# Optimization experiments

Hardware: AMD Instinct MI355X
Metric: run time of the kernel (lower is better)

Reference implementation:

```python
import jax, jax.numpy as jnp
import numpy as np

B, N, D, E, R, K = 4, 2048, 1024, 8, 256, 2


def setup_inputs() -> dict:
    key = jax.random.key(0)
    ks = jax.random.split(key, 5)
    scale = 0.02
    return {
        "x": jax.random.normal(ks[0], (B, N, D), dtype=jnp.float32),
        "gate_w": jax.random.normal(ks[1], (D, E), dtype=jnp.float32) * scale,
        "Wu": jax.random.normal(ks[2], (E, D, R), dtype=jnp.float32) * scale,
        "Wv": jax.random.normal(ks[3], (E, D, R), dtype=jnp.float32) * scale,
        "Wo": jax.random.normal(ks[4], (E, R, D), dtype=jnp.float32) * scale,
    }


def reference(x, gate_w, Wu, Wv, Wo):
    # Router: top-k over expert logits, softmax over the selected k logits.
    logits = jnp.einsum("bnd,de->bne", x, gate_w)          # [B,N,E]
    topv, topi = jax.lax.top_k(logits, K)                    # [B,N,K]
    w = jax.nn.softmax(topv, axis=-1)                        # [B,N,K]

    # Dense all-expert SwiGLU (matches reference semantics: every expert
    # computed for every token, then gathered by top-k index).
    u = jnp.einsum("bnd,edr->bner", x, Wu)                  # [B,N,E,R]
    v = jnp.einsum("bnd,edr->bner", x, Wv)                  # [B,N,E,R]
    s = jax.nn.silu(u) * v                                   # [B,N,E,R]
    Y = jnp.einsum("bner,erd->bned", s, Wo)                 # [B,N,E,D]

    # Gather the k selected experts per token and combine with gate weights.
    y_sel = jnp.take_along_axis(Y, topi[..., None], axis=2)  # [B,N,K,D]
    out = jnp.einsum("bnkd,bnk->bnd", y_sel, w)             # [B,N,D]
    return out
```

## Files before the change

kernel.cpp:

```cpp
#include <hip/hip_runtime.h>
#include <math.h>

#define BN 8192
#define DIM 1024
#define NE 8
#define RR 256

using bf16x8 = __attribute__((ext_vector_type(8))) short;
using f32x4  = __attribute__((ext_vector_type(4))) float;

#define GLD16(g, l) __builtin_amdgcn_global_load_lds(                      \
    (const __attribute__((address_space(1))) void*)(g),                    \
    (__attribute__((address_space(3))) void*)(l), 16, 0, 0)

__device__ inline unsigned short f2bf(float f) {
    unsigned int u = __float_as_uint(f);
    u = (u + 0x7fffu + ((u >> 16) & 1u)) >> 16;
    return (unsigned short)u;
}
__device__ inline float bf2f(unsigned short h) {
    unsigned int u = ((unsigned int)h) << 16;
    return __uint_as_float(u);
}

__global__ __launch_bounds__(256) void k_router3(const float* __restrict__ x,
                                                 const float* __restrict__ gwT,
                                                 int* __restrict__ topi,
                                                 float* __restrict__ topw,
                                                 unsigned short* __restrict__ xb,
                                                 int* __restrict__ counts) {
    __shared__ float gws[NE * DIM];
    __shared__ int bc[NE];
    int tid = threadIdx.x;
    {
        const float4* src = (const float4*)gwT;
        float4* dst = (float4*)gws;
#pragma unroll
        for (int i = 0; i < 8; ++i)
            dst[tid + i * 256] = src[tid + i * 256];
    }
    if (tid < NE) bc[tid] = 0;

    int wid  = (blockIdx.x * blockDim.x + tid) >> 6;
    int lane = tid & 63;
    const float* xp = x + (size_t)wid * DIM + lane * 4;
    unsigned short* xbp = xb + (size_t)wid * DIM + lane * 4;

    float4 xva[4];
#pragma unroll
    for (int k = 0; k < 4; ++k) xva[k] = *(const float4*)(xp + k * 256);

    __syncthreads();

    float4 acc[NE];
#pragma unroll
    for (int e = 0; e < NE; ++e) acc[e] = float4{0.f, 0.f, 0.f, 0.f};
#pragma unroll
    for (int k = 0; k < 4; ++k) {
        float4 xv = xva[k];
#pragma unroll
        for (int e = 0; e < NE; ++e) {
            float4 gv = *(const float4*)(gws + e * DIM + k * 256 + lane * 4);
            acc[e].x += xv.x * gv.x; acc[e].y += xv.y * gv.y;
            acc[e].z += xv.z * gv.z; acc[e].w += xv.w * gv.w;
        }
    }

#pragma unroll
    for (int k = 0; k < 4; ++k) {
        float4 xv = xva[k];
        ushort4 us = { f2bf(xv.x), f2bf(xv.y), f2bf(xv.z), f2bf(xv.w) };
        *(ushort4*)(xbp + k * 256) = us;
    }

    float lg[NE];
#pragma unroll
    for (int e = 0; e < NE; ++e)
        lg[e] = (acc[e].x + acc[e].y) + (acc[e].z + acc[e].w);
#pragma unroll
    for (int off = 32; off; off >>= 1) {
#pragma unroll
        for (int e = 0; e < NE; ++e) lg[e] += __shfl_xor(lg[e], off, 64);
    }
    if (lane == 0) {
        float best = lg[0]; int bi = 0;
#pragma unroll
        for (int e = 1; e < NE; ++e) if (lg[e] > best) { best = lg[e]; bi = e; }
        float sec = -3.4e38f; int si = 0;
#pragma unroll
        for (int e = 0; e < NE; ++e) if (e != bi && lg[e] > sec) { sec = lg[e]; si = e; }
        float p  = __expf(sec - best);
        float w0 = 1.f / (1.f + p);
        float w1 = p * w0;
        topi[wid * 2 + 0] = bi;  topw[wid * 2 + 0] = w0;
        topi[wid * 2 + 1] = si;  topw[wid * 2 + 1] = w1;
        atomicAdd(&bc[bi], 1);
        atomicAdd(&bc[si], 1);
    }
    __syncthreads();
    if (tid < NE) {
        int c = bc[tid];
        if (c) atomicAdd(&counts[tid], c);
    }
}

__global__ __launch_bounds__(256) void k_fill2(const int* __restrict__ topi,
                                               const float* __restrict__ topw,
                                               const int* __restrict__ counts,
                                               int* __restrict__ fill,
                                               int* __restrict__ btok,
                                               float* __restrict__ bw,
                                               int* __restrict__ slotOf) {
    int tid = threadIdx.x;
    int i = blockIdx.x * 256 + tid;
    int w = tid >> 6, lane = tid & 63;
    int e = topi[i];
    float wt = topw[i];

    __shared__ int waveCnt[4][NE];
    __shared__ int wavePre[4][NE];
    __shared__ int baseSh[NE];
    __shared__ int offSh[NE];

    int myrank = 0;
    unsigned long long lt = (1ull << lane) - 1ull;
#pragma unroll
    for (int j = 0; j < NE; ++j) {
        unsigned long long m = __ballot(e == j);
        if (e == j) myrank = __popcll(m & lt);
        if (lane == 0) waveCnt[w][j] = __popcll(m);
    }
    if (tid == 0) {
        int acc = 0;
#pragma unroll
        for (int j = 0; j < NE; ++j) { offSh[j] = acc; acc += counts[j]; }
    }
    __syncthreads();
    if (tid < NE) {
        int j = tid, acc = 0;
#pragma unroll
        for (int ww = 0; ww < 4; ++ww) { wavePre[ww][j] = acc; acc += waveCnt[ww][j]; }
        baseSh[j] = atomicAdd(&fill[j], acc);
    }
    __syncthreads();
    int slot = offSh[e] + baseSh[e] + wavePre[w][e] + myrank;
    btok[slot] = i >> 1;
    bw[slot]   = wt;
    slotOf[i]  = slot;
}

__global__ __launch_bounds__(256) void k_cvt3(const float* __restrict__ Wu,
                                              const float* __restrict__ Wv,
                                              const float* __restrict__ Wo,
                                              const float* __restrict__ gw,
                                              unsigned short* __restrict__ Wub,
                                              unsigned short* __restrict__ Wvb,
                                              unsigned short* __restrict__ Wob,
                                              float* __restrict__ gwT) {
    int z = blockIdx.y;
    int tile = blockIdx.x;
    if (z == 24) {
        if (tile < 32) {
            int i = tile * 256 + threadIdx.x;
            float v = gw[i];
            int d = i >> 3, e = i & 7;
            gwT[e * DIM + d] = v;
        }
        return;
    }
    int which = z >> 3, e = z & 7;
    const float* in; unsigned short* out;
    int M, N, n0, m0;
    if (which < 2) {
        M = DIM; N = RR;
        n0 = (tile & 7) * 32;  m0 = (tile >> 3) * 32;
        in = which ? Wv : Wu;  out = which ? Wvb : Wub;
    } else {
        M = RR; N = DIM;
        n0 = (tile & 31) * 32; m0 = (tile >> 5) * 32;
        in = Wo; out = Wob;
    }
    __shared__ float t[32][33];
    int tx = threadIdx.x & 31, ty = threadIdx.x >> 5;
    const float* inE = in + (size_t)e * M * N;
    unsigned short* outE = out + (size_t)e * M * N;
#pragma unroll
    for (int i = ty; i < 32; i += 8)
        t[i][tx] = inE[(size_t)(m0 + i) * N + n0 + tx];
    __syncthreads();
#pragma unroll
    for (int i = ty; i < 32; i += 8)
        outE[(size_t)(n0 + i) * M + m0 + tx] = f2bf(t[tx][i]);
}

__device__ inline bool decode_tile(const int* __restrict__ counts, int mt_lin,
                                   int& e, int& start, int& nt) {
    int acc = 0, tacc = 0;
    e = -1;
    int t0 = 0, ne = 0;
#pragma unroll
    for (int j = 0; j < NE; ++j) {
        int cj = counts[j];
        int tj = (cj + 127) >> 7;
        if (e < 0 && mt_lin < tacc + tj) {
            e = j; t0 = (mt_lin - tacc) * 128; start = acc + t0; ne = cj;
        }
        tacc += tj; acc += cj;
    }
    if (e < 0) return false;
    nt = min(128, ne - t0);
    return true;
}

__global__ __launch_bounds__(256, 2) void k_uv(
        const unsigned short* __restrict__ xb,
        const unsigned short* __restrict__ Wub,
        const unsigned short* __restrict__ Wvb,
        const int* __restrict__ counts,
        const int* __restrict__ btok,
        const float* __restrict__ bw,
        unsigned short* __restrict__ Sbuf) {
    int bid = blockIdx.x;
    int lt  = (bid & 7) * 68 + (bid >> 3);
    int rt  = lt & 3;
    int mt_lin = lt >> 2;
    int e, start, nt;
    if (!decode_tile(counts, mt_lin, e, start, nt)) return;

    int tid = threadIdx.x;
    int w = tid >> 6, lane = tid & 63;
    int m16 = lane & 15, quad = lane >> 4;
    int wm = w & 1, wn = w >> 1;

    __shared__ unsigned short As[128][64];
    __shared__ unsigned short Bs[128][64];
    __shared__ int   tokL[128];
    __shared__ float gwL[128];

    if (tid < 128) {
        tokL[tid] = (tid < nt) ? btok[start + tid] : btok[start];
        gwL[tid]  = (tid < nt) ? bw[start + tid] : 0.f;
    }
    __syncthreads();

    int rc0 = rt * 64;
    const unsigned short* WuE = Wub + (size_t)e * RR * DIM;
    const unsigned short* WvE = Wvb + (size_t)e * RR * DIM;

    const unsigned short* aS[4];
    const unsigned short* bS[4];
    int dstOff[4];
#pragma unroll
    for (int i = 0; i < 4; ++i) {
        int chunk = w * 4 + i;
        int row = chunk * 8 + (lane >> 3);
        int js  = (lane & 7) ^ (row & 7);
        aS[i] = xb + (size_t)tokL[row] * DIM + js * 8;
        bS[i] = ((row < 64) ? (WuE + (size_t)(rc0 + row) * DIM)
                            : (WvE + (size_t)(rc0 + row - 64) * DIM)) + js * 8;
        dstOff[i] = chunk * 1024;
    }
    auto* asb = (__attribute__((address_space(3))) char*)&As[0][0];
    auto* bsb = (__attribute__((address_space(3))) char*)&Bs[0][0];
    const char* Ab = (const char*)&As[0][0];
    const char* Bb = (const char*)&Bs[0][0];

    f32x4 accU[4][2], accV[4][2];
    f32x4 zz = {0.f, 0.f, 0.f, 0.f};
#pragma unroll
    for (int mt = 0; mt < 4; ++mt)
#pragma unroll
        for (int nl = 0; nl < 2; ++nl) { accU[mt][nl] = zz; accV[mt][nl] = zz; }

    for (int kt = 0; kt < 16; ++kt) {
        if (kt) __syncthreads();
#pragma unroll
        for (int i = 0; i < 4; ++i) {
            GLD16(aS[i] + kt * 64, asb + dstOff[i]);
            GLD16(bS[i] + kt * 64, bsb + dstOff[i]);
        }
        __syncthreads();
#pragma unroll
        for (int ks = 0; ks < 2; ++ks) {
            bf16x8 a[4], bu[2], bv[2];
#pragma unroll
            for (int mt = 0; mt < 4; ++mt) {
                int r = wm * 64 + mt * 16 + m16;
                int u = (ks * 4 + quad) ^ (r & 7);
                a[mt] = *(const bf16x8*)(Ab + r * 128 + u * 16);
            }
#pragma unroll
            for (int nl = 0; nl < 2; ++nl) {
                int r = wn * 32 + nl * 16 + m16;
                int u = (ks * 4 + quad) ^ (r & 7);
                bu[nl] = *(const bf16x8*)(Bb + r * 128 + u * 16);
                bv[nl] = *(const bf16x8*)(Bb + (r + 64) * 128 + u * 16);
            }
#pragma unroll
            for (int nl = 0; nl < 2; ++nl)
#pragma unroll
                for (int mt = 0; mt < 4; ++mt) {
                    accU[mt][nl] = __builtin_amdgcn_mfma_f32_16x16x32_bf16(a[mt], bu[nl], accU[mt][nl], 0, 0, 0);
                    accV[mt][nl] = __builtin_amdgcn_mfma_f32_16x16x32_bf16(a[mt], bv[nl], accV[mt][nl], 0, 0, 0);
                }
        }
    }

#pragma unroll
    for (int mt = 0; mt < 4; ++mt)
#pragma unroll
        for (int nl = 0; nl < 2; ++nl)
#pragma unroll
            for (int reg = 0; reg < 4; ++reg) {
                int trow = wm * 64 + mt * 16 + quad * 4 + reg;
                int rcol = rc0 + wn * 32 + nl * 16 + m16;
                float u = accU[mt][nl][reg], v = accV[mt][nl][reg];
                float s = (u / (1.f + __expf(-u))) * v * gwL[trow];
                if (trow < nt)
                    Sbuf[(size_t)(start + trow) * RR + rcol] = f2bf(s);
            }
}

__global__ __launch_bounds__(256, 2) void k_down(
        const unsigned short* __restrict__ Sbuf,
        const unsigned short* __restrict__ Wob,
        const int* __restrict__ counts,
        const int* __restrict__ btok,
        unsigned short* __restrict__ ybuf,
        float* __restrict__ out) {
    int bid = blockIdx.x;
    int lt  = (bid & 7) * 136 + (bid >> 3);
    int nd = lt & 7;
    int mt_lin = lt >> 3;
    int e, start, nt;
    if (!decode_tile(counts, mt_lin, e, start, nt)) return;

    int tid = threadIdx.x;
    int w = tid >> 6, lane = tid & 63;
    int m16 = lane & 15, quad = lane >> 4;
    int wm = w & 1, wn = w >> 1;

    __shared__ unsigned short As[128][64];
    __shared__ unsigned short Bs[128][64];
    __shared__ int tokL[128];

    if (tid < 128)
        tokL[tid] = (tid < nt) ? btok[start + tid] : btok[start];
    __syncthreads();

    const unsigned short* WoE = Wob + (size_t)e * DIM * RR;

    const unsigned short* aS[4];
    const unsigned short* bS[4];
    int dstOff[4];
#pragma unroll
    for (int i = 0; i < 4; ++i) {
        int chunk = w * 4 + i;
        int row = chunk * 8 + (lane >> 3);
        int js  = (lane & 7) ^ (row & 7);
        aS[i] = Sbuf + (size_t)(start + row) * RR + js * 8;
        bS[i] = WoE + (size_t)(nd * 128 + row) * RR + js * 8;
        dstOff[i] = chunk * 1024;
    }
    auto* asb = (__attribute__((address_space(3))) char*)&As[0][0];
    auto* bsb = (__attribute__((address_space(3))) char*)&Bs[0][0];
    const char* Ab = (const char*)&As[0][0];
    const char* Bb = (const char*)&Bs[0][0];

    f32x4 acc[4][4];
    f32x4 zz = {0.f, 0.f, 0.f, 0.f};
#pragma unroll
    for (int mt = 0; mt < 4; ++mt)
#pragma unroll
        for (int nl = 0; nl < 4; ++nl) acc[mt][nl] = zz;

    for (int kt = 0; kt < 4; ++kt) {
        if (kt) __syncthreads();
#pragma unroll
        for (int i = 0; i < 4; ++i) {
            GLD16(aS[i] + kt * 64, asb + dstOff[i]);
            GLD16(bS[i] + kt * 64, bsb + dstOff[i]);
        }
        __syncthreads();
#pragma unroll
        for (int ks = 0; ks < 2; ++ks) {
            bf16x8 a[4], b[4];
#pragma unroll
            for (int mt = 0; mt < 4; ++mt) {
                int r = wm * 64 + mt * 16 + m16;
                int u = (ks * 4 + quad) ^ (r & 7);
                a[mt] = *(const bf16x8*)(Ab + r * 128 + u * 16);
            }
#pragma unroll
            for (int nl = 0; nl < 4; ++nl) {
                int r = wn * 64 + nl * 16 + m16;
                int u = (ks * 4 + quad) ^ (r & 7);
                b[nl] = *(const bf16x8*)(Bb + r * 128 + u * 16);
            }
#pragma unroll
            for (int nl = 0; nl < 4; ++nl)
#pragma unroll
                for (int mt = 0; mt < 4; ++mt)
                    acc[mt][nl] = __builtin_amdgcn_mfma_f32_16x16x32_bf16(a[mt], b[nl], acc[mt][nl], 0, 0, 0);
        }
    }

    if (ybuf) {
#pragma unroll
        for (int mt = 0; mt < 4; ++mt)
#pragma unroll
            for (int nl = 0; nl < 4; ++nl)
#pragma unroll
                for (int reg = 0; reg < 4; ++reg) {
                    int srow = wm * 64 + mt * 16 + quad * 4 + reg;
                    int d    = nd * 128 + wn * 64 + nl * 16 + m16;
                    if (srow < nt)
                        ybuf[(size_t)(start + srow) * DIM + d] = f2bf(acc[mt][nl][reg]);
                }
    } else {
#pragma unroll
        for (int mt = 0; mt < 4; ++mt)
#pragma unroll
            for (int nl = 0; nl < 4; ++nl)
#pragma unroll
                for (int reg = 0; reg < 4; ++reg) {
                    int srow = wm * 64 + mt * 16 + quad * 4 + reg;
                    int d    = nd * 128 + wn * 64 + nl * 16 + m16;
                    if (srow < nt)
                        atomicAdd(&out[(size_t)tokL[srow] * DIM + d], acc[mt][nl][reg]);
                }
    }
}

__global__ __launch_bounds__(256) void k_combine(const unsigned short* __restrict__ ybuf,
                                                 const int* __restrict__ slotOf,
                                                 float* __restrict__ out) {
    int t   = blockIdx.x;
    int seg = threadIdx.x;
    int s0 = slotOf[t * 2 + 0];
    int s1 = slotOf[t * 2 + 1];
    ushort4 a4 = *(const ushort4*)(ybuf + (size_t)s0 * DIM + seg * 4);
    ushort4 b4 = *(const ushort4*)(ybuf + (size_t)s1 * DIM + seg * 4);
    float4 r = { bf2f(a4.x) + bf2f(b4.x), bf2f(a4.y) + bf2f(b4.y),
                 bf2f(a4.z) + bf2f(b4.z), bf2f(a4.w) + bf2f(b4.w) };
    *(float4*)(out + (size_t)t * DIM + seg * 4) = r;
}

extern "C" void kernel_launch(void* const* d_in, const int* in_sizes, int n_in,
                              void* d_out, int out_size, void* d_ws, size_t ws_size,
                              hipStream_t stream) {
    const float* x  = (const float*)d_in[0];
    const float* gw = (const float*)d_in[1];
    const float* Wu = (const float*)d_in[2];
    const float* Wv = (const float*)d_in[3];
    const float* Wo = (const float*)d_in[4];
    float* out = (float*)d_out;

    int*   wsi     = (int*)d_ws;
    int*   counts  = wsi + 0;
    int*   fill    = wsi + 16;
    int*   topi    = wsi + 48;
    float* topw    = (float*)(wsi + 48 + 16384);
    int*   btok    = wsi + 48 + 32768;
    float* bw      = (float*)(wsi + 48 + 49152);
    int*   slotOf  = wsi + 48 + 65536;
    float* gwT     = (float*)((char*)d_ws + 327872);

    const size_t off_xb  = 393216;
    const size_t off_wub = off_xb  + (size_t)BN * DIM * 2;
    const size_t off_wvb = off_wub + (size_t)NE * RR * DIM * 2;
    const size_t off_wob = off_wvb + (size_t)NE * RR * DIM * 2;
    const size_t off_sb  = off_wob + (size_t)NE * DIM * RR * 2;
    const size_t off_yb  = off_sb  + (size_t)(BN * 2 + 128) * RR * 2;
    const size_t need_yb = off_yb  + (size_t)BN * 2 * DIM * 2;

    unsigned short* xb   = (unsigned short*)((char*)d_ws + off_xb);
    unsigned short* Wub  = (unsigned short*)((char*)d_ws + off_wub);
    unsigned short* Wvb  = (unsigned short*)((char*)d_ws + off_wvb);
    unsigned short* Wob  = (unsigned short*)((char*)d_ws + off_wob);
    unsigned short* Sbuf = (unsigned short*)((char*)d_ws + off_sb);
    bool use_ybuf = (ws_size >= need_yb);
    unsigned short* ybuf = use_ybuf ? (unsigned short*)((char*)d_ws + off_yb) : nullptr;

    hipMemsetAsync(wsi, 0, 192, stream);

    k_cvt3<<<dim3(256, 25), 256, 0, stream>>>(Wu, Wv, Wo, gw, Wub, Wvb, Wob, gwT);
    k_router3<<<dim3(BN / 4), 256, 0, stream>>>(x, gwT, topi, topw, xb, counts);
    k_fill2<<<dim3(BN * 2 / 256), 256, 0, stream>>>(topi, topw, counts, fill,
                                                    btok, bw, slotOf);

    if (!use_ybuf)
        hipMemsetAsync(d_out, 0, (size_t)BN * DIM * sizeof(float), stream);

    k_uv<<<dim3(544), 256, 0, stream>>>(xb, Wub, Wvb, counts, btok, bw, Sbuf);
    k_down<<<dim3(1088), 256, 0, stream>>>(Sbuf, Wob, counts, btok, ybuf, out);
    if (use_ybuf)
        k_combine<<<dim3(BN), 256, 0, stream>>>(ybuf, slotOf, out);
}
```

Measured before the change: 189.3 us.

## Halve k_uv rank tile to double grid; fold workspace zeroing into cvt kernel

The up/gate GEMM kernel now covers 32 rank columns per block instead of 64, which doubles the grid from 544 to 1088 blocks and halves the per-block B tile and accumulator count. The aim is better occupancy and load balance across CUs, at the cost of re-reading the gathered activation tile twice as often and a lower MFMA-to-load ratio. Separately, the 192-byte workspace memset is replaced by zeroing inside the weight-conversion kernel, which removes one API call and its launch.

```diff
diff --git a/kernel.cpp b/kernel.cpp
--- a/kernel.cpp
+++ b/kernel.cpp
@@ -156,7 +156,8 @@
                                               unsigned short* __restrict__ Wub,
                                               unsigned short* __restrict__ Wvb,
                                               unsigned short* __restrict__ Wob,
-                                              float* __restrict__ gwT) {
+                                              float* __restrict__ gwT,
+                                              int* __restrict__ wsz) {
     int z = blockIdx.y;
     int tile = blockIdx.x;
     if (z == 24) {
@@ -165,6 +166,8 @@
             float v = gw[i];
             int d = i >> 3, e = i & 7;
             gwT[e * DIM + d] = v;
+        } else if (tile == 32 && threadIdx.x < 48) {
+            wsz[threadIdx.x] = 0;
         }
         return;
     }
@@ -221,9 +224,9 @@
         const float* __restrict__ bw,
         unsigned short* __restrict__ Sbuf) {
     int bid = blockIdx.x;
-    int lt  = (bid & 7) * 68 + (bid >> 3);
-    int rt  = lt & 3;
-    int mt_lin = lt >> 2;
+    int lt  = (bid & 7) * 136 + (bid >> 3);
+    int rt  = lt & 7;
+    int mt_lin = lt >> 3;
     int e, start, nt;
     if (!decode_tile(counts, mt_lin, e, start, nt)) return;
 
@@ -233,7 +236,7 @@
     int wm = w & 1, wn = w >> 1;
 
     __shared__ unsigned short As[128][64];
-    __shared__ unsigned short Bs[128][64];
+    __shared__ unsigned short Bs[64][64];
     __shared__ int   tokL[128];
     __shared__ float gwL[128];
 
@@ -243,82 +246,85 @@
     }
     __syncthreads();
 
-    int rc0 = rt * 64;
+    int rc0 = rt * 32;
     const unsigned short* WuE = Wub + (size_t)e * RR * DIM;
     const unsigned short* WvE = Wvb + (size_t)e * RR * DIM;
 
-    const unsigned short* aS[4];
-    const unsigned short* bS[4];
-    int dstOff[4];
-#pragma unroll
-    for (int i = 0; i < 4; ++i) {
-        int chunk = w * 4 + i;
-        int row = chunk * 8 + (lane >> 3);
-        int js  = (lane & 7) ^ (row & 7);
-        aS[i] = xb + (size_t)tokL[row] * DIM + js * 8;
-        bS[i] = ((row < 64) ? (WuE + (size_t)(rc0 + row) * DIM)
-                            : (WvE + (size_t)(rc0 + row - 64) * DIM)) + js * 8;
-        dstOff[i] = chunk * 1024;
+    const unsigned short* src[6];
+    int off[6];
+    bool isA[6];
+#pragma unroll
+    for (int i = 0; i < 6; ++i) {
+        int chunk = w * 6 + i;
+        if (chunk < 16) {
+            int row = chunk * 8 + (lane >> 3);
+            int js  = (lane & 7) ^ (row & 7);
+            src[i] = xb + (size_t)tokL[row] * DIM + js * 8;
+            off[i] = chunk * 1024;
+            isA[i] = true;
+        } else {
+            int row = (chunk - 16) * 8 + (lane >> 3);
+            int js  = (lane & 7) ^ (row & 7);
+            src[i] = ((row < 32) ? (WuE + (size_t)(rc0 + row) * DIM)
+                                 : (WvE + (size_t)(rc0 + row - 32) * DIM)) + js * 8;
+            off[i] = (chunk - 16) * 1024;
+            isA[i] = false;
+        }
     }
     auto* asb = (__attribute__((address_space(3))) char*)&As[0][0];
     auto* bsb = (__attribute__((address_space(3))) char*)&Bs[0][0];
     const char* Ab = (const char*)&As[0][0];
     const char* Bb = (const char*)&Bs[0][0];
 
-    f32x4 accU[4][2], accV[4][2];
+    f32x4 accU[4], accV[4];
     f32x4 zz = {0.f, 0.f, 0.f, 0.f};
 #pragma unroll
-    for (int mt = 0; mt < 4; ++mt)
-#pragma unroll
-        for (int nl = 0; nl < 2; ++nl) { accU[mt][nl] = zz; accV[mt][nl] = zz; }
+    for (int mt = 0; mt < 4; ++mt) { accU[mt] = zz; accV[mt] = zz; }
 
     for (int kt = 0; kt < 16; ++kt) {
         if (kt) __syncthreads();
 #pragma unroll
-        for (int i = 0; i < 4; ++i) {
-            GLD16(aS[i] + kt * 64, asb + dstOff[i]);
-            GLD16(bS[i] + kt * 64, bsb + dstOff[i]);
+        for (int i = 0; i < 6; ++i) {
+            if (isA[i]) GLD16(src[i] + kt * 64, asb + off[i]);
+            else        GLD16(src[i] + kt * 64, bsb + off[i]);
         }
         __syncthreads();
 #pragma unroll
         for (int ks = 0; ks < 2; ++ks) {
-            bf16x8 a[4], bu[2], bv[2];
+            bf16x8 a[4], bu, bv;
 #pragma unroll
             for (int mt = 0; mt < 4; ++mt) {
                 int r = wm * 64 + mt * 16 + m16;
                 int u = (ks * 4 + quad) ^ (r & 7);
                 a[mt] = *(const bf16x8*)(Ab + r * 128 + u * 16);
             }
-#pragma unroll
-            for (int nl = 0; nl < 2; ++nl) {
-                int r = wn * 32 + nl * 16 + m16;
+            {
+                int r = wn * 16 + m16;
                 int u = (ks * 4 + quad) ^ (r & 7);
-                bu[nl] = *(const bf16x8*)(Bb + r * 128 + u * 16);
-                bv[nl] = *(const bf16x8*)(Bb + (r + 64) * 128 + u * 16);
+                bu = *(const bf16x8*)(Bb + r * 128 + u * 16);
+                int r2 = r + 32;
+                int u2 = (ks * 4 + quad) ^ (r2 & 7);
+                bv = *(const bf16x8*)(Bb + r2 * 128 + u2 * 16);
             }
 #pragma unroll
-            for (int nl = 0; nl < 2; ++nl)
-#pragma unroll
-                for (int mt = 0; mt < 4; ++mt) {
-                    accU[mt][nl] = __builtin_amdgcn_mfma_f32_16x16x32_bf16(a[mt], bu[nl], accU[mt][nl], 0, 0, 0);
-                    accV[mt][nl] = __builtin_amdgcn_mfma_f32_16x16x32_bf16(a[mt], bv[nl], accV[mt][nl], 0, 0, 0);
-                }
+            for (int mt = 0; mt < 4; ++mt) {
+                accU[mt] = __builtin_amdgcn_mfma_f32_16x16x32_bf16(a[mt], bu, accU[mt], 0, 0, 0);
+                accV[mt] = __builtin_amdgcn_mfma_f32_16x16x32_bf16(a[mt], bv, accV[mt], 0, 0, 0);
+            }
         }
     }
 
 #pragma unroll
     for (int mt = 0; mt < 4; ++mt)
 #pragma unroll
-        for (int nl = 0; nl < 2; ++nl)
-#pragma unroll
-            for (int reg = 0; reg < 4; ++reg) {
-                int trow = wm * 64 + mt * 16 + quad * 4 + reg;
-                int rcol = rc0 + wn * 32 + nl * 16 + m16;
-                float u = accU[mt][nl][reg], v = accV[mt][nl][reg];
-                float s = (u / (1.f + __expf(-u))) * v * gwL[trow];
-                if (trow < nt)
-                    Sbuf[(size_t)(start + trow) * RR + rcol] = f2bf(s);
-            }
+        for (int reg = 0; reg < 4; ++reg) {
+            int trow = wm * 64 + mt * 16 + quad * 4 + reg;
+            int rcol = rc0 + wn * 16 + m16;
+            float u = accU[mt][reg], v = accV[mt][reg];
+            float s = (u / (1.f + __expf(-u))) * v * gwL[trow];
+            if (trow < nt)
+                Sbuf[(size_t)(start + trow) * RR + rcol] = f2bf(s);
+        }
 }
 
 __global__ __launch_bounds__(256, 2) void k_down(
@@ -482,9 +488,8 @@
     bool use_ybuf = (ws_size >= need_yb);
     unsigned short* ybuf = use_ybuf ? (unsigned short*)((char*)d_ws + off_yb) : nullptr;
 
-    hipMemsetAsync(wsi, 0, 192, stream);
-
-    k_cvt3<<<dim3(256, 25), 256, 0, stream>>>(Wu, Wv, Wo, gw, Wub, Wvb, Wob, gwT);
+    k_cvt3<<<dim3(256, 25), 256, 0, stream>>>(Wu, Wv, Wo, gw, Wub, Wvb, Wob,
+                                              gwT, wsi);
     k_router3<<<dim3(BN / 4), 256, 0, stream>>>(x, gwT, topi, topw, xb, counts);
     k_fill2<<<dim3(BN * 2 / 256), 256, 0, stream>>>(topi, topw, counts, fill,
                                                     btok, bw, slotOf);
@@ -492,7 +497,7 @@
     if (!use_ybuf)
         hipMemsetAsync(d_out, 0, (size_t)BN * DIM * sizeof(float), stream);
 
-    k_uv<<<dim3(544), 256, 0, stream>>>(xb, Wub, Wvb, counts, btok, bw, Sbuf);
+    k_uv<<<dim3(1088), 256, 0, stream>>>(xb, Wub, Wvb, counts, btok, bw, Sbuf);
     k_down<<<dim3(1088), 256, 0, stream>>>(Sbuf, Wob, counts, btok, ybuf, out);
     if (use_ybuf)
         k_combine<<<dim3(BN), 256, 0, stream>>>(ybuf, slotOf, out);
```

Result: no change. 191.2 us (+1.0%).

## Double-buffer LDS K-tiles in up and down GEMMs; fold workspace memset into convert kernel

Applied to the files above, without the earlier changes.

Both expert GEMM kernels now use two half-width (K=32) LDS buffers and issue the next tile's global-to-LDS loads before computing on the current one, with one barrier per iteration. The aim is to overlap global load latency with MFMA work in place of the old load-sync-compute-sync sequence. The swizzle changes to match the 64-byte rows, and each iteration now has half the MFMA work per barrier. The separate hipMemsetAsync of the counter workspace is dropped and the zeroing is done inside k_cvt3 to save a launch.

```diff
diff --git a/kernel.cpp b/kernel.cpp
--- a/kernel.cpp
+++ b/kernel.cpp
@@ -156,7 +156,8 @@
                                               unsigned short* __restrict__ Wub,
                                               unsigned short* __restrict__ Wvb,
                                               unsigned short* __restrict__ Wob,
-                                              float* __restrict__ gwT) {
+                                              float* __restrict__ gwT,
+                                              int* __restrict__ wsz) {
     int z = blockIdx.y;
     int tile = blockIdx.x;
     if (z == 24) {
@@ -165,6 +166,8 @@
             float v = gw[i];
             int d = i >> 3, e = i & 7;
             gwT[e * DIM + d] = v;
+        } else if (tile == 32 && threadIdx.x < 48) {
+            wsz[threadIdx.x] = 0;
         }
         return;
     }
@@ -232,8 +235,8 @@
     int m16 = lane & 15, quad = lane >> 4;
     int wm = w & 1, wn = w >> 1;
 
-    __shared__ unsigned short As[128][64];
-    __shared__ unsigned short Bs[128][64];
+    __shared__ unsigned short As[2][128][32];
+    __shared__ unsigned short Bs[2][128][32];
     __shared__ int   tokL[128];
     __shared__ float gwL[128];
 
@@ -247,23 +250,36 @@
     const unsigned short* WuE = Wub + (size_t)e * RR * DIM;
     const unsigned short* WvE = Wvb + (size_t)e * RR * DIM;
 
-    const unsigned short* aS[4];
-    const unsigned short* bS[4];
-    int dstOff[4];
+    const unsigned short* src[4];
+    int off[4];
+    bool isA[4];
 #pragma unroll
     for (int i = 0; i < 4; ++i) {
         int chunk = w * 4 + i;
-        int row = chunk * 8 + (lane >> 3);
-        int js  = (lane & 7) ^ (row & 7);
-        aS[i] = xb + (size_t)tokL[row] * DIM + js * 8;
-        bS[i] = ((row < 64) ? (WuE + (size_t)(rc0 + row) * DIM)
-                            : (WvE + (size_t)(rc0 + row - 64) * DIM)) + js * 8;
-        dstOff[i] = chunk * 1024;
-    }
-    auto* asb = (__attribute__((address_space(3))) char*)&As[0][0];
-    auto* bsb = (__attribute__((address_space(3))) char*)&Bs[0][0];
-    const char* Ab = (const char*)&As[0][0];
-    const char* Bb = (const char*)&Bs[0][0];
+        int row = (chunk & 7) * 16 + (lane >> 2);
+        int js  = (lane & 3) ^ ((row >> 1) & 3);
+        if (chunk < 8) {
+            src[i] = xb + (size_t)tokL[row] * DIM + js * 8;
+            isA[i] = true;
+        } else {
+            src[i] = ((row < 64) ? (WuE + (size_t)(rc0 + row) * DIM)
+                                 : (WvE + (size_t)(rc0 + row - 64) * DIM)) + js * 8;
+            isA[i] = false;
+        }
+        off[i] = (chunk & 7) * 1024;
+    }
+    auto* asb = (__attribute__((address_space(3))) char*)&As[0][0][0];
+    auto* bsb = (__attribute__((address_space(3))) char*)&Bs[0][0][0];
+    const char* Ab = (const char*)&As[0][0][0];
+    const char* Bb = (const char*)&Bs[0][0][0];
+
+    auto stage = [&](int buf, int kt) {
+#pragma unroll
+        for (int i = 0; i < 4; ++i) {
+            if (isA[i]) GLD16(src[i] + kt * 32, asb + buf * 8192 + off[i]);
+            else        GLD16(src[i] + kt * 32, bsb + buf * 8192 + off[i]);
+        }
+    };
 
     f32x4 accU[4][2], accV[4][2];
     f32x4 zz = {0.f, 0.f, 0.f, 0.f};
@@ -272,38 +288,35 @@
 #pragma unroll
         for (int nl = 0; nl < 2; ++nl) { accU[mt][nl] = zz; accV[mt][nl] = zz; }
 
-    for (int kt = 0; kt < 16; ++kt) {
-        if (kt) __syncthreads();
-#pragma unroll
-        for (int i = 0; i < 4; ++i) {
-            GLD16(aS[i] + kt * 64, asb + dstOff[i]);
-            GLD16(bS[i] + kt * 64, bsb + dstOff[i]);
-        }
+    stage(0, 0);
+    __syncthreads();
+    for (int kt = 0; kt < 32; ++kt) {
+        const int cur = kt & 1;
+        if (kt < 31) stage(cur ^ 1, kt + 1);
+        bf16x8 a[4], bu[2], bv[2];
+#pragma unroll
+        for (int mt = 0; mt < 4; ++mt) {
+            int r = wm * 64 + mt * 16 + m16;
+            int u = quad ^ ((r >> 1) & 3);
+            a[mt] = *(const bf16x8*)(Ab + cur * 8192 + r * 64 + u * 16);
+        }
+#pragma unroll
+        for (int nl = 0; nl < 2; ++nl) {
+            int r = wn * 32 + nl * 16 + m16;
+            int u = quad ^ ((r >> 1) & 3);
+            bu[nl] = *(const bf16x8*)(Bb + cur * 8192 + r * 64 + u * 16);
+            int r2 = r + 64;
+            int u2 = quad ^ ((r2 >> 1) & 3);
+            bv[nl] = *(const bf16x8*)(Bb + cur * 8192 + r2 * 64 + u2 * 16);
+        }
+#pragma unroll
+        for (int nl = 0; nl < 2; ++nl)
+#pragma unroll
+            for (int mt = 0; mt < 4; ++mt) {
+                accU[mt][nl] = __builtin_amdgcn_mfma_f32_16x16x32_bf16(a[mt], bu[nl], accU[mt][nl], 0, 0, 0);
+                accV[mt][nl] = __builtin_amdgcn_mfma_f32_16x16x32_bf16(a[mt], bv[nl], accV[mt][nl], 0, 0, 0);
+            }
         __syncthreads();
-#pragma unroll
-        for (int ks = 0; ks < 2; ++ks) {
-            bf16x8 a[4], bu[2], bv[2];
-#pragma unroll
-            for (int mt = 0; mt < 4; ++mt) {
-                int r = wm * 64 + mt * 16 + m16;
-                int u = (ks * 4 + quad) ^ (r & 7);
-                a[mt] = *(const bf16x8*)(Ab + r * 128 + u * 16);
-            }
-#pragma unroll
-            for (int nl = 0; nl < 2; ++nl) {
-                int r = wn * 32 + nl * 16 + m16;
-                int u = (ks * 4 + quad) ^ (r & 7);
-                bu[nl] = *(const bf16x8*)(Bb + r * 128 + u * 16);
-                bv[nl] = *(const bf16x8*)(Bb + (r + 64) * 128 + u * 16);
-            }
-#pragma unroll
-            for (int nl = 0; nl < 2; ++nl)
-#pragma unroll
-                for (int mt = 0; mt < 4; ++mt) {
-                    accU[mt][nl] = __builtin_amdgcn_mfma_f32_16x16x32_bf16(a[mt], bu[nl], accU[mt][nl], 0, 0, 0);
-                    accV[mt][nl] = __builtin_amdgcn_mfma_f32_16x16x32_bf16(a[mt], bv[nl], accV[mt][nl], 0, 0, 0);
-                }
-        }
     }
 
 #pragma unroll
@@ -340,8 +353,8 @@
     int m16 = lane & 15, quad = lane >> 4;
     int wm = w & 1, wn = w >> 1;
 
-    __shared__ unsigned short As[128][64];
-    __shared__ unsigned short Bs[128][64];
+    __shared__ unsigned short As[2][128][32];
+    __shared__ unsigned short Bs[2][128][32];
     __shared__ int tokL[128];
 
     if (tid < 128)
@@ -350,22 +363,35 @@
 
     const unsigned short* WoE = Wob + (size_t)e * DIM * RR;
 
-    const unsigned short* aS[4];
-    const unsigned short* bS[4];
-    int dstOff[4];
+    const unsigned short* src[4];
+    int off[4];
+    bool isA[4];
 #pragma unroll
     for (int i = 0; i < 4; ++i) {
         int chunk = w * 4 + i;
-        int row = chunk * 8 + (lane >> 3);
-        int js  = (lane & 7) ^ (row & 7);
-        aS[i] = Sbuf + (size_t)(start + row) * RR + js * 8;
-        bS[i] = WoE + (size_t)(nd * 128 + row) * RR + js * 8;
-        dstOff[i] = chunk * 1024;
-    }
-    auto* asb = (__attribute__((address_space(3))) char*)&As[0][0];
-    auto* bsb = (__attribute__((address_space(3))) char*)&Bs[0][0];
-    const char* Ab = (const char*)&As[0][0];
-    const char* Bb = (const char*)&Bs[0][0];
+        int row = (chunk & 7) * 16 + (lane >> 2);
+        int js  = (lane & 3) ^ ((row >> 1) & 3);
+        if (chunk < 8) {
+            src[i] = Sbuf + (size_t)(start + row) * RR + js * 8;
+            isA[i] = true;
+        } else {
+            src[i] = WoE + (size_t)(nd * 128 + row) * RR + js * 8;
+            isA[i] = false;
+        }
+        off[i] = (chunk & 7) * 1024;
+    }
+    auto* asb = (__attribute__((address_space(3))) char*)&As[0][0][0];
+    auto* bsb = (__attribute__((address_space(3))) char*)&Bs[0][0][0];
+    const char* Ab = (const char*)&As[0][0][0];
+    const char* Bb = (const char*)&Bs[0][0][0];
+
+    auto stage = [&](int buf, int kt) {
+#pragma unroll
+        for (int i = 0; i < 4; ++i) {
+            if (isA[i]) GLD16(src[i] + kt * 32, asb + buf * 8192 + off[i]);
+            else        GLD16(src[i] + kt * 32, bsb + buf * 8192 + off[i]);
+        }
+    };
 
     f32x4 acc[4][4];
     f32x4 zz = {0.f, 0.f, 0.f, 0.f};
@@ -374,35 +400,30 @@
 #pragma unroll
         for (int nl = 0; nl < 4; ++nl) acc[mt][nl] = zz;
 
-    for (int kt = 0; kt < 4; ++kt) {
-        if (kt) __syncthreads();
-#pragma unroll
-        for (int i = 0; i < 4; ++i) {
-            GLD16(aS[i] + kt * 64, asb + dstOff[i]);
-            GLD16(bS[i] + kt * 64, bsb + dstOff[i]);
-        }
+    stage(0, 0);
+    __syncthreads();
+    for (int kt = 0; kt < 8; ++kt) {
+        const int cur = kt & 1;
+        if (kt < 7) stage(cur ^ 1, kt + 1);
+        bf16x8 a[4], b[4];
+#pragma unroll
+        for (int mt = 0; mt < 4; ++mt) {
+            int r = wm * 64 + mt * 16 + m16;
+            int u = quad ^ ((r >> 1) & 3);
+            a[mt] = *(const bf16x8*)(Ab + cur * 8192 + r * 64 + u * 16);
+        }
+#pragma unroll
+        for (int nl = 0; nl < 4; ++nl) {
+            int r = wn * 64 + nl * 16 + m16;
+            int u = quad ^ ((r >> 1) & 3);
+            b[nl] = *(const bf16x8*)(Bb + cur * 8192 + r * 64 + u * 16);
+        }
+#pragma unroll
+        for (int nl = 0; nl < 4; ++nl)
+#pragma unroll
+            for (int mt = 0; mt < 4; ++mt)
+                acc[mt][nl] = __builtin_amdgcn_mfma_f32_16x16x32_bf16(a[mt], b[nl], acc[mt][nl], 0, 0, 0);
         __syncthreads();
-#pragma unroll
-        for (int ks = 0; ks < 2; ++ks) {
-            bf16x8 a[4], b[4];
-#pragma unroll
-            for (int mt = 0; mt < 4; ++mt) {
-                int r = wm * 64 + mt * 16 + m16;
-                int u = (ks * 4 + quad) ^ (r & 7);
-                a[mt] = *(const bf16x8*)(Ab + r * 128 + u * 16);
-            }
-#pragma unroll
-            for (int nl = 0; nl < 4; ++nl) {
-                int r = wn * 64 + nl * 16 + m16;
-                int u = (ks * 4 + quad) ^ (r & 7);
-                b[nl] = *(const bf16x8*)(Bb + r * 128 + u * 16);
-            }
-#pragma unroll
-            for (int nl = 0; nl < 4; ++nl)
-#pragma unroll
-                for (int mt = 0; mt < 4; ++mt)
-                    acc[mt][nl] = __builtin_amdgcn_mfma_f32_16x16x32_bf16(a[mt], b[nl], acc[mt][nl], 0, 0, 0);
-        }
     }
 
     if (ybuf) {
@@ -482,9 +503,8 @@
     bool use_ybuf = (ws_size >= need_yb);
     unsigned short* ybuf = use_ybuf ? (unsigned short*)((char*)d_ws + off_yb) : nullptr;
 
-    hipMemsetAsync(wsi, 0, 192, stream);
-
-    k_cvt3<<<dim3(256, 25), 256, 0, stream>>>(Wu, Wv, Wo, gw, Wub, Wvb, Wob, gwT);
+    k_cvt3<<<dim3(256, 25), 256, 0, stream>>>(Wu, Wv, Wo, gw, Wub, Wvb, Wob,
+                                              gwT, wsi);
     k_router3<<<dim3(BN / 4), 256, 0, stream>>>(x, gwT, topi, topw, xb, counts);
     k_fill2<<<dim3(BN * 2 / 256), 256, 0, stream>>>(topi, topw, counts, fill,
                                                     btok, bw, slotOf);
```

New measurement: 191.0 us. About the same (+0.9%).
